# Performance work log

Hardware: AMD Instinct MI355X
Metric: run time of the kernel (lower is better)

## Reference

```python
import jax, jax.numpy as jnp
import numpy as np

TOP_K = 2
CAPACITY_FACTOR = 1.0
ALIGNMENT = 4  # 4 * sharded_count(=1) * a2a_ffn_overlap_degree(=1)
EPS = 1e-7


def setup_inputs() -> dict:
    key = jax.random.key(0)
    ks = jax.random.split(key, 5)
    S, M, H, E = 4096, 1024, 4096, 8
    x = jax.random.normal(ks[0], (S, M), jnp.float32)
    wg = jax.random.normal(ks[1], (M, E), jnp.float32) / np.sqrt(M)
    fc1_w = jax.random.normal(ks[2], (E, M, H), jnp.float32) / np.sqrt(M)
    fc1_b = jnp.zeros((E, H), jnp.float32)
    fc2_w = jax.random.normal(ks[3], (E, H, M), jnp.float32) / np.sqrt(H)
    fc2_b = jnp.zeros((E, M), jnp.float32)
    return {"x": x, "wg": wg, "fc1_w": fc1_w, "fc1_b": fc1_b,
            "fc2_w": fc2_w, "fc2_b": fc2_b}


def _moe(x, wg, fc1_w, fc1_b, fc2_w, fc2_b):
    S, M = x.shape
    E = wg.shape[1]
    K = TOP_K
    # static capacity, aligned (Tutel extract_critical)
    C = -(-(K * S) // E)
    C = int(np.ceil(C * CAPACITY_FACTOR))
    C = ((C + ALIGNMENT - 1) // ALIGNMENT) * ALIGNMENT

    # --- gating (eval mode: no gate noise) ---
    logits = x @ wg                                  # [S, E]
    scores = jax.nn.softmax(logits, axis=1)
    topk_vals, topk_ids = jax.lax.top_k(scores, K)   # [S, K]

    # --- per-expert slot locations (sequential over k-levels) ---
    masks = jax.nn.one_hot(topk_ids, E, dtype=jnp.int32)   # [S, K, E]
    locs = []
    offset = jnp.zeros((E,), jnp.int32)
    for i in range(K):
        m = masks[:, i]                               # [S, E]
        loc_i = jnp.cumsum(m, axis=0) - 1 + offset[None, :]
        locs.append(jnp.sum(loc_i * m, axis=1))       # [S]
        offset = offset + jnp.sum(m, axis=0)
    loc = jnp.stack(locs, axis=1)                     # [S, K]

    # --- normalize gates over selected experts ---
    denom = jnp.maximum(jnp.sum(topk_vals, axis=1, keepdims=True), EPS)
    gates = topk_vals / denom                         # [S, K]

    valid = (loc >= 0) & (loc < C)                    # capacity drop
    flat = topk_ids * C + jnp.clip(loc, 0, C - 1)     # [S, K] -> index into E*C

    # --- encode / dispatch (postscore: unscaled) ---
    xk = jnp.where(valid[..., None], x[:, None, :], 0.0)        # [S, K, M]
    y = jnp.zeros((E * C, M), x.dtype).at[flat.reshape(-1)].add(xk.reshape(-1, M))
    y = y.reshape(E, C, M)

    # --- grouped expert FFN ---
    h = jax.nn.relu(jnp.einsum('ecm,emh->ech', y, fc1_w) + fc1_b[:, None, :])
    yo = jnp.einsum('ech,ehm->ecm', h, fc2_w) + fc2_b[:, None, :]

    # --- combine / decode (postscore: scale by gates) ---
    g = jnp.where(valid, gates, 0.0)                   # [S, K]
    gathered = yo.reshape(E * C, M)[flat.reshape(-1)].reshape(S, K, M)
    out = jnp.einsum('sk,skm->sm', g, gathered)        # [S, M]

    # --- gshard aux loss ---
    me = jnp.mean(scores, axis=0)                      # [E]
    ce = jnp.mean(jax.nn.one_hot(topk_ids[:, 0], E, dtype=scores.dtype), axis=0)
    l_aux = jnp.sum(me * ce) * E
    return out, l_aux


def reference(x, wg, fc1_w, fc1_b, fc2_w, fc2_b):
    return _moe(x, wg, fc1_w, fc1_b, fc2_w, fc2_b)
```

## Files before the change

kernel.cpp:

```cpp
#include <hip/hip_runtime.h>
#include <stdint.h>

#define S_TOK 4096
#define MDIM  1024
#define HDIM  4096
#define NEXP  8
#define CAP   1024

typedef __attribute__((ext_vector_type(4))) float f4;
typedef __attribute__((ext_vector_type(8))) short short8;
typedef __attribute__((ext_vector_type(4))) unsigned short us4;
typedef __attribute__((ext_vector_type(8))) unsigned short us8;

__device__ __forceinline__ unsigned short f2bf(float f) {
  union { float f; unsigned int u; } v; v.f = f;
  unsigned int u = v.u;
  unsigned int r = (u + 0x7FFFu + ((u >> 16) & 1u)) >> 16;
  return (unsigned short)r;
}

__device__ __forceinline__ void async16(const unsigned short* gp, unsigned short* lp_wave_base) {
  __builtin_amdgcn_global_load_lds(
      (const __attribute__((address_space(1))) unsigned int*)gp,
      (__attribute__((address_space(3))) unsigned int*)lp_wave_base,
      16, 0, 0);
}

__global__ __launch_bounds__(256) void gating_kernel(
    const float* __restrict__ x, const float* __restrict__ wg,
    float* __restrict__ scores, int* __restrict__ topk_ids,
    float* __restrict__ gates)
{
  int wave = threadIdx.x >> 6, lane = threadIdx.x & 63;
  int s = blockIdx.x * 4 + wave;
  const float* xs = x + (size_t)s * MDIM;
  float acc[8];
#pragma unroll
  for (int e = 0; e < 8; ++e) acc[e] = 0.f;
#pragma unroll
  for (int j = 0; j < 4; ++j) {
    f4 xv = *(const f4*)(xs + j * 256 + lane * 4);
#pragma unroll
    for (int i = 0; i < 4; ++i) {
      int m = j * 256 + lane * 4 + i;
      const f4* w = (const f4*)(wg + (size_t)m * 8);
      f4 w0 = w[0], w1 = w[1];
      acc[0] += xv[i] * w0[0]; acc[1] += xv[i] * w0[1];
      acc[2] += xv[i] * w0[2]; acc[3] += xv[i] * w0[3];
      acc[4] += xv[i] * w1[0]; acc[5] += xv[i] * w1[1];
      acc[6] += xv[i] * w1[2]; acc[7] += xv[i] * w1[3];
    }
  }
#pragma unroll
  for (int e = 0; e < 8; ++e) {
    float v = acc[e];
    for (int off = 32; off; off >>= 1) v += __shfl_xor(v, off, 64);
    acc[e] = v;
  }
  if (lane == 0) {
    float mx = acc[0];
#pragma unroll
    for (int e = 1; e < 8; ++e) mx = fmaxf(mx, acc[e]);
    float p[8], tot = 0.f;
#pragma unroll
    for (int e = 0; e < 8; ++e) { p[e] = expf(acc[e] - mx); tot += p[e]; }
    float inv = 1.f / tot;
#pragma unroll
    for (int e = 0; e < 8; ++e) { p[e] *= inv; scores[s * 8 + e] = p[e]; }
    int i0 = 0;
#pragma unroll
    for (int e = 1; e < 8; ++e) if (p[e] > p[i0]) i0 = e;
    int i1 = -1;
#pragma unroll
    for (int e = 0; e < 8; ++e) {
      if (e == i0) continue;
      if (i1 < 0 || p[e] > p[i1]) i1 = e;
    }
    float v0 = p[i0], v1 = p[i1];
    float den = fmaxf(v0 + v1, 1e-7f);
    topk_ids[s * 2] = i0; topk_ids[s * 2 + 1] = i1;
    gates[s * 2] = v0 / den; gates[s * 2 + 1] = v1 / den;
  }
}

__global__ __launch_bounds__(1024) void assign_kernel(
    const int* __restrict__ topk_ids, const float* __restrict__ gates,
    int* __restrict__ row_src, float* __restrict__ row_gate)
{
  __shared__ unsigned long long sc0[1024], sc1[1024];
  int t = threadIdx.x;
#pragma unroll
  for (int j = 0; j < 8; ++j) row_src[t * 8 + j] = -1;

  int e8[8];
  unsigned long long c0 = 0, c1 = 0;
  int base = t * 8;
#pragma unroll
  for (int j = 0; j < 8; ++j) {
    int i = base + j;
    int k = i >> 12, s = i & 4095;
    int e = topk_ids[s * 2 + k];
    e8[j] = e;
    if (e < 4) c0 += 1ull << (16 * e); else c1 += 1ull << (16 * (e - 4));
  }
  sc0[t] = c0; sc1[t] = c1;
  __syncthreads();
  for (int off = 1; off < 1024; off <<= 1) {
    unsigned long long a0 = 0, a1 = 0;
    if (t >= off) { a0 = sc0[t - off]; a1 = sc1[t - off]; }
    __syncthreads();
    sc0[t] += a0; sc1[t] += a1;
    __syncthreads();
  }
  unsigned long long r0 = 0, r1 = 0;
  if (t > 0) { r0 = sc0[t - 1]; r1 = sc1[t - 1]; }
#pragma unroll
  for (int j = 0; j < 8; ++j) {
    int i = base + j;
    int k = i >> 12, s = i & 4095;
    int e = e8[j];
    int loc = (e < 4) ? (int)((r0 >> (16 * e)) & 0xFFFFull)
                      : (int)((r1 >> (16 * (e - 4))) & 0xFFFFull);
    if (e < 4) r0 += 1ull << (16 * e); else r1 += 1ull << (16 * (e - 4));
    if (loc < CAP) {
      int flat = e * CAP + loc;
      row_src[flat] = s;
      row_gate[flat] = gates[s * 2 + k];
    }
  }
}

__global__ __launch_bounds__(256) void dispatch_kernel(
    const float* __restrict__ x, const int* __restrict__ row_src,
    unsigned short* __restrict__ y)
{
  int r = blockIdx.x * 2 + (threadIdx.x >> 7);
  int s = row_src[r];
  int m0 = (threadIdx.x & 127) * 8;
  us8 o;
  if (s >= 0) {
    f4 v0 = *(const f4*)(x + (size_t)s * MDIM + m0);
    f4 v1 = *(const f4*)(x + (size_t)s * MDIM + m0 + 4);
#pragma unroll
    for (int i = 0; i < 4; ++i) { o[i] = f2bf(v0[i]); o[4 + i] = f2bf(v1[i]); }
  } else {
#pragma unroll
    for (int i = 0; i < 8; ++i) o[i] = 0;
  }
  *(us8*)(y + (size_t)r * MDIM + m0) = o;
}

__global__ __launch_bounds__(256) void convT_kernel(
    const float* __restrict__ in, unsigned short* __restrict__ out,
    int R, int Cc)
{
  __shared__ float tile[64 * 68];
  int e = blockIdx.z;
  int c0 = blockIdx.x * 64, r0 = blockIdx.y * 64;
  int t = threadIdx.x;
  const float* ine = in + (size_t)e * R * Cc;
  unsigned short* oute = out + (size_t)e * Cc * R;

  int cg = t & 15, rr = t >> 4;
#pragma unroll
  for (int p = 0; p < 4; ++p) {
    int r = rr + 16 * p;
    f4 v = __builtin_nontemporal_load(
        (const f4*)(ine + (size_t)(r0 + r) * Cc + c0 + cg * 4));
    *(f4*)&tile[r * 68 + cg * 4] = v;
  }
  __syncthreads();
  int c = t >> 3, rb = t & 7;
#pragma unroll
  for (int p = 0; p < 2; ++p) {
    int cc = c + 32 * p;
    us8 o;
#pragma unroll
    for (int i = 0; i < 8; ++i) o[i] = f2bf(tile[(rb * 8 + i) * 68 + cc]);
    *(us8*)(oute + (size_t)(c0 + cc) * R + r0 + rb * 8) = o;
  }
}

__global__ __launch_bounds__(512, 4) void gemm_bt(
    const unsigned short* __restrict__ A, const unsigned short* __restrict__ Bt,
    const float* __restrict__ bias, unsigned short* __restrict__ Cout,
    int RA, int N, int K, int relu, int gxmask, int gxshift,
    int fuse, const int* __restrict__ row_src, const float* __restrict__ row_gate,
    float* __restrict__ out)
{
  int lin = blockIdx.x;
  int e = lin & 7;
  int tt = lin >> 3;
  int bCol = (tt & gxmask) * 128;
  int bRow = (tt >> gxshift) * 128;

  const unsigned short* Ae = A  + (size_t)e * RA * K;
  const unsigned short* Be = Bt + (size_t)e * N  * K;
  const float* be = bias + (size_t)e * N;

  __shared__ __align__(16) unsigned short LDSbuf[16384];
  unsigned short* Atile[2] = { LDSbuf,        LDSbuf + 4096 };
  unsigned short* Btile[2] = { LDSbuf + 8192, LDSbuf + 12288 };

  int tid = threadIdx.x;
  int lane = tid & 63, wave = tid >> 6;
  int wr = wave >> 2, wc = wave & 3;
  int q = lane >> 4, r16 = lane & 15;

  f4 acc[4][2] = {};

  for (int k0 = 0; k0 < K; k0 += 64) {
#pragma unroll
    for (int ks = 0; ks < 2; ++ks) {
      int ci = wave * 64 + lane;
      int row = ci >> 2, c8 = (ci & 3) * 8;
      async16(Ae + (size_t)(bRow + row) * K + k0 + ks * 32 + c8, Atile[ks] + wave * 512);
      async16(Be + (size_t)(bCol + row) * K + k0 + ks * 32 + c8, Btile[ks] + wave * 512);
    }
    __syncthreads();
#pragma unroll
    for (int ks = 0; ks < 2; ++ks) {
      short8 af[4], bf[2];
#pragma unroll
      for (int mt = 0; mt < 4; ++mt)
        af[mt] = *(const short8*)&Atile[ks][(wr * 64 + mt * 16 + r16) * 32 + q * 8];
#pragma unroll
      for (int nt = 0; nt < 2; ++nt)
        bf[nt] = *(const short8*)&Btile[ks][(wc * 32 + nt * 16 + r16) * 32 + q * 8];
#pragma unroll
      for (int mt = 0; mt < 4; ++mt)
#pragma unroll
        for (int nt = 0; nt < 2; ++nt)
          acc[mt][nt] = __builtin_amdgcn_mfma_f32_16x16x32_bf16(af[mt], bf[nt], acc[mt][nt], 0, 0, 0);
    }
    __syncthreads();
  }

  float bv[2];
#pragma unroll
  for (int nt = 0; nt < 2; ++nt) bv[nt] = be[bCol + wc * 32 + nt * 16 + r16];

  if (!fuse) {
    unsigned short* ep = LDSbuf + wave * 2048;
#pragma unroll
    for (int mt = 0; mt < 4; ++mt)
#pragma unroll
      for (int nt = 0; nt < 2; ++nt)
#pragma unroll
        for (int r = 0; r < 4; ++r) {
          float v = acc[mt][nt][r] + bv[nt];
          if (relu) v = fmaxf(v, 0.f);
          ep[(mt * 16 + q * 4 + r) * 32 + nt * 16 + r16] = f2bf(v);
        }
#pragma unroll
    for (int pass = 0; pass < 4; ++pass) {
      int row = pass * 16 + (lane >> 2);
      int seg = lane & 3;
      us8 v = *(const us8*)&ep[row * 32 + seg * 8];
      *(us8*)&Cout[((size_t)e * RA + bRow + wr * 64 + row) * N + bCol + wc * 32 + seg * 8] = v;
    }
  } else {
#pragma unroll
    for (int mt = 0; mt < 4; ++mt)
#pragma unroll
      for (int r = 0; r < 4; ++r) {
        int grow = e * RA + bRow + wr * 64 + mt * 16 + q * 4 + r;
        int s = row_src[grow];
        if (s < 0) continue;
        float g = row_gate[grow];
#pragma unroll
        for (int nt = 0; nt < 2; ++nt) {
          float v = acc[mt][nt][r] + bv[nt];
          atomicAdd(out + (size_t)s * N + bCol + wc * 32 + nt * 16 + r16, g * v);
        }
      }
  }
}

__global__ __launch_bounds__(256) void aux_kernel(
    const float* __restrict__ scores, const int* __restrict__ topk_ids,
    float* __restrict__ laux_out)
{
  __shared__ float red[256];
  __shared__ float msum[8], csum[8];
  int t = threadIdx.x;
  float me[8], ce[8];
#pragma unroll
  for (int e = 0; e < 8; ++e) { me[e] = 0.f; ce[e] = 0.f; }
  for (int s = t; s < S_TOK; s += 256) {
#pragma unroll
    for (int e = 0; e < 8; ++e) me[e] += scores[s * 8 + e];
    int top = topk_ids[s * 2];
#pragma unroll
    for (int e = 0; e < 8; ++e) ce[e] += (top == e) ? 1.f : 0.f;
  }
  for (int e = 0; e < 8; ++e) {
    red[t] = me[e]; __syncthreads();
    for (int off = 128; off; off >>= 1) { if (t < off) red[t] += red[t + off]; __syncthreads(); }
    if (t == 0) msum[e] = red[0];
    __syncthreads();
  }
  for (int e = 0; e < 8; ++e) {
    red[t] = ce[e]; __syncthreads();
    for (int off = 128; off; off >>= 1) { if (t < off) red[t] += red[t + off]; __syncthreads(); }
    if (t == 0) csum[e] = red[0];
    __syncthreads();
  }
  if (t == 0) {
    float l = 0.f;
#pragma unroll
    for (int e = 0; e < 8; ++e)
      l += (msum[e] / (float)S_TOK) * (csum[e] / (float)S_TOK);
    laux_out[0] = l * (float)NEXP;
  }
}

extern "C" void kernel_launch(void* const* d_in, const int* in_sizes, int n_in,
                              void* d_out, int out_size, void* d_ws, size_t ws_size,
                              hipStream_t stream) {
  const float* x     = (const float*)d_in[0];
  const float* wg    = (const float*)d_in[1];
  const float* fc1_w = (const float*)d_in[2];
  const float* fc1_b = (const float*)d_in[3];
  const float* fc2_w = (const float*)d_in[4];
  const float* fc2_b = (const float*)d_in[5];
  float* out = (float*)d_out;

  char* ws = (char*)d_ws;
  size_t off = 0;
  auto alloc = [&](size_t b) { size_t o = off; off += (b + 255) & ~(size_t)255; return o; };
  unsigned short* fc1T = (unsigned short*)(ws + alloc((size_t)NEXP * HDIM * MDIM * 2));
  unsigned short* fc2T = (unsigned short*)(ws + alloc((size_t)NEXP * MDIM * HDIM * 2));
  unsigned short* y    = (unsigned short*)(ws + alloc((size_t)NEXP * CAP * MDIM * 2));
  unsigned short* h    = (unsigned short*)(ws + alloc((size_t)NEXP * CAP * HDIM * 2));
  float* scores        = (float*)(ws + alloc((size_t)S_TOK * 8 * 4));
  int*   topk          = (int*)(ws + alloc((size_t)S_TOK * 2 * 4));
  float* gates         = (float*)(ws + alloc((size_t)S_TOK * 2 * 4));
  int*   row_src       = (int*)(ws + alloc((size_t)NEXP * CAP * 4));
  float* row_gate      = (float*)(ws + alloc((size_t)NEXP * CAP * 4));

  hipMemsetAsync(d_out, 0, (size_t)out_size * 4, stream);

  convT_kernel<<<dim3(HDIM / 64, MDIM / 64, NEXP), 256, 0, stream>>>(fc1_w, fc1T, MDIM, HDIM);
  convT_kernel<<<dim3(MDIM / 64, HDIM / 64, NEXP), 256, 0, stream>>>(fc2_w, fc2T, HDIM, MDIM);

  gating_kernel<<<dim3(S_TOK / 4), 256, 0, stream>>>(x, wg, scores, topk, gates);
  assign_kernel<<<dim3(1), 1024, 0, stream>>>(topk, gates, row_src, row_gate);
  dispatch_kernel<<<dim3(NEXP * CAP / 2), 256, 0, stream>>>(x, row_src, y);

  gemm_bt<<<dim3(2048), 512, 0, stream>>>(y, fc1T, fc1_b, h, CAP, HDIM, MDIM, 1, 31, 5,
                                          0, nullptr, nullptr, nullptr);

  gemm_bt<<<dim3(512), 512, 0, stream>>>(h, fc2T, fc2_b, nullptr, CAP, MDIM, HDIM, 0, 7, 3,
                                         1, row_src, row_gate, out);

  aux_kernel<<<dim3(1), 256, 0, stream>>>(scores, topk, out + (size_t)S_TOK * MDIM);
}
```

Before: 519.7 us.

## Double-buffer LDS tiles in grouped expert GEMM to overlap loads with MFMA

The K-loop of the expert GEMM becomes a ping-pong pipeline over two LDS buffers. The next 64-wide K slice is issued with async global-to-LDS loads while MFMAs run on the current slice, which also cuts the barriers per slice from two to one. Shared memory per block doubles from 32 KB to 64 KB. With the launch bound of 4 blocks per CU, that may lower how many blocks fit on a CU.

Result: no change. 513.5 us (-1.2%).

```diff
diff --git a/kernel.cpp b/kernel.cpp
--- a/kernel.cpp
+++ b/kernel.cpp
@@ -198,59 +198,80 @@
   const unsigned short* Be = Bt + (size_t)e * N  * K;
   const float* be = bias + (size_t)e * N;
 
-  __shared__ __align__(16) unsigned short LDSbuf[16384];
-  unsigned short* Atile[2] = { LDSbuf,        LDSbuf + 4096 };
-  unsigned short* Btile[2] = { LDSbuf + 8192, LDSbuf + 12288 };
+  __shared__ __align__(16) unsigned short LDSbuf[32768];
+  unsigned short* bufA = LDSbuf;
+  unsigned short* bufB = LDSbuf + 16384;
 
   int tid = threadIdx.x;
   int lane = tid & 63, wave = tid >> 6;
   int wr = wave >> 2, wc = wave & 3;
   int q = lane >> 4, r16 = lane & 15;
 
+  int ci = wave * 64 + lane;
+  int srow = ci >> 2, sc8 = (ci & 3) * 8;
+  const unsigned short* agp = Ae + (size_t)(bRow + srow) * K + sc8;
+  const unsigned short* bgp = Be + (size_t)(bCol + srow) * K + sc8;
+
   f4 acc[4][2] = {};
 
-  for (int k0 = 0; k0 < K; k0 += 64) {
+  auto STAGE = [&](int k0, unsigned short* buf) {
 #pragma unroll
     for (int ks = 0; ks < 2; ++ks) {
-      int ci = wave * 64 + lane;
-      int row = ci >> 2, c8 = (ci & 3) * 8;
-      async16(Ae + (size_t)(bRow + row) * K + k0 + ks * 32 + c8, Atile[ks] + wave * 512);
-      async16(Be + (size_t)(bCol + row) * K + k0 + ks * 32 + c8, Btile[ks] + wave * 512);
-    }
-    __syncthreads();
+      async16(agp + k0 + ks * 32, buf + ks * 4096 + wave * 512);
+      async16(bgp + k0 + ks * 32, buf + 8192 + ks * 4096 + wave * 512);
+    }
+  };
+  auto COMPUTE = [&](const unsigned short* buf) {
 #pragma unroll
     for (int ks = 0; ks < 2; ++ks) {
       short8 af[4], bf[2];
 #pragma unroll
       for (int mt = 0; mt < 4; ++mt)
-        af[mt] = *(const short8*)&Atile[ks][(wr * 64 + mt * 16 + r16) * 32 + q * 8];
+        af[mt] = *(const short8*)&buf[ks * 4096 + (wr * 64 + mt * 16 + r16) * 32 + q * 8];
 #pragma unroll
       for (int nt = 0; nt < 2; ++nt)
-        bf[nt] = *(const short8*)&Btile[ks][(wc * 32 + nt * 16 + r16) * 32 + q * 8];
+        bf[nt] = *(const short8*)&buf[8192 + ks * 4096 + (wc * 32 + nt * 16 + r16) * 32 + q * 8];
 #pragma unroll
       for (int mt = 0; mt < 4; ++mt)
 #pragma unroll
         for (int nt = 0; nt < 2; ++nt)
           acc[mt][nt] = __builtin_amdgcn_mfma_f32_16x16x32_bf16(af[mt], bf[nt], acc[mt][nt], 0, 0, 0);
     }
-    __syncthreads();
-  }
+  };
+
+  int nt = K >> 6;
+  STAGE(0, bufA);
+  __syncthreads();
+  int t = 0;
+  for (; t < nt - 2; t += 2) {
+    STAGE((t + 1) << 6, bufB);
+    COMPUTE(bufA);
+    __syncthreads();
+    STAGE((t + 2) << 6, bufA);
+    COMPUTE(bufB);
+    __syncthreads();
+  }
+  STAGE((nt - 1) << 6, bufB);
+  COMPUTE(bufA);
+  __syncthreads();
+  COMPUTE(bufB);
+  __syncthreads();
 
   float bv[2];
 #pragma unroll
-  for (int nt = 0; nt < 2; ++nt) bv[nt] = be[bCol + wc * 32 + nt * 16 + r16];
+  for (int nt2 = 0; nt2 < 2; ++nt2) bv[nt2] = be[bCol + wc * 32 + nt2 * 16 + r16];
 
   if (!fuse) {
     unsigned short* ep = LDSbuf + wave * 2048;
 #pragma unroll
     for (int mt = 0; mt < 4; ++mt)
 #pragma unroll
-      for (int nt = 0; nt < 2; ++nt)
+      for (int nt2 = 0; nt2 < 2; ++nt2)
 #pragma unroll
         for (int r = 0; r < 4; ++r) {
-          float v = acc[mt][nt][r] + bv[nt];
+          float v = acc[mt][nt2][r] + bv[nt2];
           if (relu) v = fmaxf(v, 0.f);
-          ep[(mt * 16 + q * 4 + r) * 32 + nt * 16 + r16] = f2bf(v);
+          ep[(mt * 16 + q * 4 + r) * 32 + nt2 * 16 + r16] = f2bf(v);
         }
 #pragma unroll
     for (int pass = 0; pass < 4; ++pass) {
@@ -269,9 +290,9 @@
         if (s < 0) continue;
         float g = row_gate[grow];
 #pragma unroll
-        for (int nt = 0; nt < 2; ++nt) {
-          float v = acc[mt][nt][r] + bv[nt];
-          atomicAdd(out + (size_t)s * N + bCol + wc * 32 + nt * 16 + r16, g * v);
+        for (int nt2 = 0; nt2 < 2; ++nt2) {
+          float v = acc[mt][nt2][r] + bv[nt2];
+          atomicAdd(out + (size_t)s * N + bCol + wc * 32 + nt2 * 16 + r16, g * v);
         }
       }
   }
```

## Pipeline expert GEMM with 4-stage async LDS ring and row-fast tile order

Applied to the files above, without the earlier changes.

Replaces the load-then-sync-then-compute loop in the grouped expert GEMM with a 4-deep ring of LDS buffers. Async global-to-LDS loads are issued three K-steps ahead, and explicit vmcnt waits plus one barrier per step replace the two __syncthreads per iteration. This is meant to hide global memory latency behind MFMA work. It also adds a rowfast flag so the fc1 GEMM walks row tiles fastest, which changes which weight tiles neighbouring blocks share in L2. LDS use per block doubles to 64KB, which may cut occupancy below the 4 blocks per CU the launch bounds request.

Result: no change. 513.8 us (-1.1%).

```diff
diff --git a/kernel.cpp b/kernel.cpp
--- a/kernel.cpp
+++ b/kernel.cpp
@@ -184,73 +184,95 @@
 __global__ __launch_bounds__(512, 4) void gemm_bt(
     const unsigned short* __restrict__ A, const unsigned short* __restrict__ Bt,
     const float* __restrict__ bias, unsigned short* __restrict__ Cout,
-    int RA, int N, int K, int relu, int gxmask, int gxshift,
+    int RA, int N, int K, int relu, int gxmask, int gxshift, int rowfast,
     int fuse, const int* __restrict__ row_src, const float* __restrict__ row_gate,
     float* __restrict__ out)
 {
   int lin = blockIdx.x;
   int e = lin & 7;
   int tt = lin >> 3;
-  int bCol = (tt & gxmask) * 128;
-  int bRow = (tt >> gxshift) * 128;
+  int i0 = tt & gxmask, i1 = tt >> gxshift;
+  int bRow, bCol;
+  if (rowfast) { bRow = i0 * 128; bCol = i1 * 128; }
+  else         { bCol = i0 * 128; bRow = i1 * 128; }
 
   const unsigned short* Ae = A  + (size_t)e * RA * K;
   const unsigned short* Be = Bt + (size_t)e * N  * K;
   const float* be = bias + (size_t)e * N;
 
-  __shared__ __align__(16) unsigned short LDSbuf[16384];
-  unsigned short* Atile[2] = { LDSbuf,        LDSbuf + 4096 };
-  unsigned short* Btile[2] = { LDSbuf + 8192, LDSbuf + 12288 };
+  __shared__ __align__(16) unsigned short LDSbuf[32768];
 
   int tid = threadIdx.x;
   int lane = tid & 63, wave = tid >> 6;
   int wr = wave >> 2, wc = wave & 3;
   int q = lane >> 4, r16 = lane & 15;
 
+  int ci = wave * 64 + lane;
+  int srow = ci >> 2, sc8 = (ci & 3) * 8;
+  const unsigned short* agp = Ae + (size_t)(bRow + srow) * K + sc8;
+  const unsigned short* bgp = Be + (size_t)(bCol + srow) * K + sc8;
+
   f4 acc[4][2] = {};
 
-  for (int k0 = 0; k0 < K; k0 += 64) {
-#pragma unroll
-    for (int ks = 0; ks < 2; ++ks) {
-      int ci = wave * 64 + lane;
-      int row = ci >> 2, c8 = (ci & 3) * 8;
-      async16(Ae + (size_t)(bRow + row) * K + k0 + ks * 32 + c8, Atile[ks] + wave * 512);
-      async16(Be + (size_t)(bCol + row) * K + k0 + ks * 32 + c8, Btile[ks] + wave * 512);
-    }
-    __syncthreads();
-#pragma unroll
-    for (int ks = 0; ks < 2; ++ks) {
-      short8 af[4], bf[2];
-#pragma unroll
-      for (int mt = 0; mt < 4; ++mt)
-        af[mt] = *(const short8*)&Atile[ks][(wr * 64 + mt * 16 + r16) * 32 + q * 8];
-#pragma unroll
-      for (int nt = 0; nt < 2; ++nt)
-        bf[nt] = *(const short8*)&Btile[ks][(wc * 32 + nt * 16 + r16) * 32 + q * 8];
-#pragma unroll
-      for (int mt = 0; mt < 4; ++mt)
-#pragma unroll
-        for (int nt = 0; nt < 2; ++nt)
-          acc[mt][nt] = __builtin_amdgcn_mfma_f32_16x16x32_bf16(af[mt], bf[nt], acc[mt][nt], 0, 0, 0);
-    }
-    __syncthreads();
-  }
+  auto STAGE = [&](int t) {
+    unsigned short* buf = LDSbuf + (t & 3) * 8192;
+    async16(agp + t * 32, buf + wave * 512);
+    async16(bgp + t * 32, buf + 4096 + wave * 512);
+  };
+  auto COMPUTE = [&](int t) {
+    const unsigned short* buf = LDSbuf + (t & 3) * 8192;
+    short8 af[4], bf[2];
+#pragma unroll
+    for (int mt = 0; mt < 4; ++mt)
+      af[mt] = *(const short8*)&buf[(wr * 64 + mt * 16 + r16) * 32 + q * 8];
+#pragma unroll
+    for (int nn = 0; nn < 2; ++nn)
+      bf[nn] = *(const short8*)&buf[4096 + (wc * 32 + nn * 16 + r16) * 32 + q * 8];
+#pragma unroll
+    for (int mt = 0; mt < 4; ++mt)
+#pragma unroll
+      for (int nn = 0; nn < 2; ++nn)
+        acc[mt][nn] = __builtin_amdgcn_mfma_f32_16x16x32_bf16(af[mt], bf[nn], acc[mt][nn], 0, 0, 0);
+  };
+
+  int ntk = K >> 5;
+  STAGE(0); STAGE(1); STAGE(2);
+  asm volatile("s_waitcnt vmcnt(4)" ::: "memory");
+  __builtin_amdgcn_s_barrier();
+  __builtin_amdgcn_sched_barrier(0);
+  for (int t = 0; t < ntk - 3; ++t) {
+    STAGE(t + 3);
+    COMPUTE(t);
+    asm volatile("s_waitcnt vmcnt(4) lgkmcnt(0)" ::: "memory");
+    __builtin_amdgcn_s_barrier();
+    __builtin_amdgcn_sched_barrier(0);
+  }
+  COMPUTE(ntk - 3);
+  asm volatile("s_waitcnt vmcnt(2) lgkmcnt(0)" ::: "memory");
+  __builtin_amdgcn_s_barrier();
+  __builtin_amdgcn_sched_barrier(0);
+  COMPUTE(ntk - 2);
+  asm volatile("s_waitcnt vmcnt(0) lgkmcnt(0)" ::: "memory");
+  __builtin_amdgcn_s_barrier();
+  __builtin_amdgcn_sched_barrier(0);
+  COMPUTE(ntk - 1);
+  __syncthreads();
 
   float bv[2];
 #pragma unroll
-  for (int nt = 0; nt < 2; ++nt) bv[nt] = be[bCol + wc * 32 + nt * 16 + r16];
+  for (int nn = 0; nn < 2; ++nn) bv[nn] = be[bCol + wc * 32 + nn * 16 + r16];
 
   if (!fuse) {
     unsigned short* ep = LDSbuf + wave * 2048;
 #pragma unroll
     for (int mt = 0; mt < 4; ++mt)
 #pragma unroll
-      for (int nt = 0; nt < 2; ++nt)
+      for (int nn = 0; nn < 2; ++nn)
 #pragma unroll
         for (int r = 0; r < 4; ++r) {
-          float v = acc[mt][nt][r] + bv[nt];
+          float v = acc[mt][nn][r] + bv[nn];
           if (relu) v = fmaxf(v, 0.f);
-          ep[(mt * 16 + q * 4 + r) * 32 + nt * 16 + r16] = f2bf(v);
+          ep[(mt * 16 + q * 4 + r) * 32 + nn * 16 + r16] = f2bf(v);
         }
 #pragma unroll
     for (int pass = 0; pass < 4; ++pass) {
@@ -269,9 +291,9 @@
         if (s < 0) continue;
         float g = row_gate[grow];
 #pragma unroll
-        for (int nt = 0; nt < 2; ++nt) {
-          float v = acc[mt][nt][r] + bv[nt];
-          atomicAdd(out + (size_t)s * N + bCol + wc * 32 + nt * 16 + r16, g * v);
+        for (int nn = 0; nn < 2; ++nn) {
+          float v = acc[mt][nn][r] + bv[nn];
+          atomicAdd(out + (size_t)s * N + bCol + wc * 32 + nn * 16 + r16, g * v);
         }
       }
   }
@@ -348,10 +370,10 @@
   assign_kernel<<<dim3(1), 1024, 0, stream>>>(topk, gates, row_src, row_gate);
   dispatch_kernel<<<dim3(NEXP * CAP / 2), 256, 0, stream>>>(x, row_src, y);
 
-  gemm_bt<<<dim3(2048), 512, 0, stream>>>(y, fc1T, fc1_b, h, CAP, HDIM, MDIM, 1, 31, 5,
+  gemm_bt<<<dim3(2048), 512, 0, stream>>>(y, fc1T, fc1_b, h, CAP, HDIM, MDIM, 1, 7, 3, 1,
                                           0, nullptr, nullptr, nullptr);
 
-  gemm_bt<<<dim3(512), 512, 0, stream>>>(h, fc2T, fc2_b, nullptr, CAP, MDIM, HDIM, 0, 7, 3,
+  gemm_bt<<<dim3(512), 512, 0, stream>>>(h, fc2T, fc2_b, nullptr, CAP, MDIM, HDIM, 0, 7, 3, 0,
                                          1, row_src, row_gate, out);
 
   aux_kernel<<<dim3(1), 256, 0, stream>>>(scores, topk, out + (size_t)S_TOK * MDIM);
```
